# Optimization experiments

Hardware: AMD Instinct MI355X
Metric: run time of the kernel (lower is better)

## Reference

```python
import jax, jax.numpy as jnp
import numpy as np

N_NODES = 100000
N_EDGES = 1600000
NFEAT = 128
NHID = 128
NCLS = 40


def _glorot(key, shape):
    fan_in, fan_out = shape[1], shape[0]
    lim = (6.0 / (fan_in + fan_out)) ** 0.5
    return jax.random.uniform(key, shape, jnp.float32, -lim, lim)


def setup_inputs() -> dict:
    key = jax.random.key(0)
    ks = jax.random.split(key, 10)
    x = jax.random.normal(ks[0], (N_NODES, NFEAT), jnp.float32)
    edge_index = jax.random.randint(ks[1], (2, N_EDGES), 0, N_NODES, jnp.int64)
    return {
        "x": x,
        "edge_index": edge_index,
        # SAGEConv layer 0: lin_l (neighbor aggr, with bias) and lin_r (root)
        "W_l0": _glorot(ks[2], (NHID, NFEAT)),
        "b_l0": jnp.zeros((NHID,), jnp.float32),
        "W_r0": _glorot(ks[3], (NHID, NFEAT)),
        # SAGEConv layer 1
        "W_l1": _glorot(ks[4], (NHID, NHID)),
        "b_l1": jnp.zeros((NHID,), jnp.float32),
        "W_r1": _glorot(ks[5], (NHID, NHID)),
        # classifier
        "W_cls": _glorot(ks[6], (NCLS, NHID)),
        "b_cls": jnp.zeros((NCLS,), jnp.float32),
    }


def _sage_conv(x, src, dst, deg_inv, W_l, b_l, W_r):
    # gather source-node features along edges, mean-aggregate at targets
    msgs = x[src]                                            # [E, d_in]
    aggr = jax.ops.segment_sum(msgs, dst, num_segments=N_NODES)  # [N, d_in]
    aggr = aggr * deg_inv[:, None]                           # mean
    # out = lin_l(aggr) + lin_r(x)
    return aggr @ W_l.T + b_l + x @ W_r.T


def reference(x, edge_index, W_l0, b_l0, W_r0, W_l1, b_l1, W_r1, W_cls, b_cls):
    src, dst = edge_index[0], edge_index[1]
    deg = jax.ops.segment_sum(jnp.ones((src.shape[0],), x.dtype), dst,
                              num_segments=N_NODES)
    deg_inv = 1.0 / jnp.maximum(deg, 1.0)

    h = jax.nn.relu(_sage_conv(x, src, dst, deg_inv, W_l0, b_l0, W_r0))
    h = jax.nn.relu(_sage_conv(h, src, dst, deg_inv, W_l1, b_l1, W_r1))
    return h @ W_cls.T + b_cls  # [N, ncls]
```

## Files before the change

kernel.cpp:

```cpp
#include <hip/hip_runtime.h>

#define NN 100000
#define NE 1600000
#define DD 128
#define NCLS_ 40
#define PAD 64
#define NPART 8
#define PSZ 12500
#define PBLK 250
#define ECHUNK 6400

typedef unsigned short u16;
typedef unsigned int u32;
typedef __attribute__((ext_vector_type(8))) short short8;
typedef __attribute__((ext_vector_type(4))) float f32x4;

static __device__ __forceinline__ u16 f2b(float f) {
  u32 u = __float_as_uint(f);
  u32 r = (u + 0x7FFFu + ((u >> 16) & 1u)) >> 16;
  return (u16)r;
}

__global__ void k_flag(const int* __restrict__ ei, int* __restrict__ flag) {
  __shared__ int nz;
  if (threadIdx.x == 0) nz = 0;
  __syncthreads();
  if (threadIdx.x < 512) {
    int w = ei[2 * threadIdx.x + 1];
    if (w != 0) atomicOr(&nz, 1);
  }
  __syncthreads();
  if (threadIdx.x == 0) flag[0] = (nz == 0) ? 1 : 0;
}

static __device__ __forceinline__ int eget_nt(const int* ei, int pos, int is64) {
  return is64 ? __builtin_nontemporal_load(ei + 2 * (size_t)pos)
              : __builtin_nontemporal_load(ei + pos);
}

__global__ __launch_bounds__(256) void k_build(
    const int* __restrict__ ei, const int* __restrict__ flag,
    int* __restrict__ cnt, int* __restrict__ csrp) {
  int is64 = flag[0];
  int g = blockIdx.x & (NPART - 1);
  int sub = blockIdx.x >> 3;
  int e0 = sub * ECHUNK;
  int lo = g * PSZ;
  for (int e = e0 + threadIdx.x; e < e0 + ECHUNK; e += 256) {
    int dst = eget_nt(ei, NE + e, is64);
    if ((u32)(dst - lo) < (u32)PSZ) {
      int src = eget_nt(ei, e, is64);
      int r = atomicAdd(&cnt[dst], 1);
      if (r < PAD) csrp[dst * PAD + r] = src;
    }
  }
}

__global__ void k_cvt4(const float* __restrict__ s, u16* __restrict__ d, int n4) {
  int i = blockIdx.x * 256 + threadIdx.x;
  if (i >= n4) return;
  float4 v = ((const float4*)s)[i];
  u32 lo = (u32)f2b(v.x) | ((u32)f2b(v.y) << 16);
  u32 hi = (u32)f2b(v.z) | ((u32)f2b(v.w) << 16);
  ((uint2*)d)[i] = make_uint2(lo, hi);
}

__global__ void k_cvtw(const float* __restrict__ w0, const float* __restrict__ w1,
                       const float* __restrict__ w2, const float* __restrict__ w3,
                       u16* __restrict__ o0, u16* __restrict__ o1,
                       u16* __restrict__ o2, u16* __restrict__ o3) {
  int i = blockIdx.x * 256 + threadIdx.x;
  int which = i >> 12, j = i & 4095;
  const float* s = which == 0 ? w0 : which == 1 ? w1 : which == 2 ? w2 : w3;
  u16* d = which == 0 ? o0 : which == 1 ? o1 : which == 2 ? o2 : o3;
  float4 v = ((const float4*)s)[j];
  u32 lo = (u32)f2b(v.x) | ((u32)f2b(v.y) << 16);
  u32 hi = (u32)f2b(v.z) | ((u32)f2b(v.w) << 16);
  ((uint2*)d)[j] = make_uint2(lo, hi);
}

__global__ void k_cvtcls(const float* __restrict__ s, u16* __restrict__ d) {
  int i = blockIdx.x * 256 + threadIdx.x;
  if (i >= 48 * DD) return;
  float v = (i < NCLS_ * DD) ? s[i] : 0.f;
  d[i] = f2b(v);
}

__global__ __launch_bounds__(256, 2) void k_aggr(
    const u16* __restrict__ in, const int* __restrict__ csrp,
    const int* __restrict__ cnt, u16* __restrict__ out) {
  int wid = blockIdx.x * 4 + (threadIdx.x >> 6);
  if (wid >= NN) return;
  int lane = threadIdx.x & 63;
  int l16 = lane & 15;
  int deg = cnt[wid];
  int nb = deg > PAD ? PAD : deg;
  const u32* in32 = (const u32*)in;
  const int* seg = csrp + (size_t)wid * PAD;
  float a0 = 0.f, a1 = 0.f;
  int full = nb >> 4;
  for (int b = 0; b < full; b++) {
    int c = seg[b * 16 + l16];
    u32 v[16];
#pragma unroll
    for (int k = 0; k < 16; k++) {
      int sk = __builtin_amdgcn_readlane(c, k);
      v[k] = in32[(size_t)sk * 64 + lane];
    }
#pragma unroll
    for (int k = 0; k < 16; k++) {
      a0 += __uint_as_float(v[k] << 16);
      a1 += __uint_as_float(v[k] & 0xFFFF0000u);
    }
  }
  int done = full << 4;
  int rem = nb - done;
  if (rem) {
    int c = seg[done + (l16 < rem ? l16 : 0)];
    u32 v[16];
#pragma unroll
    for (int k = 0; k < 16; k++) {
      if (k < rem) {
        int sk = __builtin_amdgcn_readlane(c, k);
        v[k] = in32[(size_t)sk * 64 + lane];
      }
    }
#pragma unroll
    for (int k = 0; k < 16; k++) {
      if (k < rem) {
        a0 += __uint_as_float(v[k] << 16);
        a1 += __uint_as_float(v[k] & 0xFFFF0000u);
      }
    }
  }
  float sc = 1.0f / (float)(deg > 1 ? deg : 1);
  a0 *= sc;
  a1 *= sc;
  u32 pk = (u32)f2b(a0) | ((u32)f2b(a1) << 16);
  ((u32*)out)[(size_t)wid * 64 + lane] = pk;
}

template <int NT, bool RELU, bool F32OUT, bool HASR>
__global__ __launch_bounds__(256) void k_layer(
    const u16* A1, const u16* A2,
    const u16* __restrict__ WL, const u16* __restrict__ WR,
    const float* __restrict__ bias, void* out, int ncols) {
  int wv = blockIdx.x * 4 + (threadIdx.x >> 6);
  int base = wv * 16;
  if (base >= NN) return;
  int lane = threadIdx.x & 63;
  int m = lane & 15, kg = lane >> 4;
  f32x4 acc[NT];
#pragma unroll
  for (int t = 0; t < NT; t++) acc[t] = (f32x4){0.f, 0.f, 0.f, 0.f};
#pragma unroll
  for (int kk = 0; kk < 4; kk++) {
    int ko = kk * 32 + kg * 8;
    short8 aA = *(const short8*)(A1 + (size_t)(base + m) * DD + ko);
    short8 aX;
    if constexpr (HASR) aX = *(const short8*)(A2 + (size_t)(base + m) * DD + ko);
#pragma unroll
    for (int t = 0; t < NT; t++) {
      short8 bL = *(const short8*)(WL + (size_t)(t * 16 + m) * DD + ko);
      acc[t] = __builtin_amdgcn_mfma_f32_16x16x32_bf16(aA, bL, acc[t], 0, 0, 0);
      if constexpr (HASR) {
        short8 bR = *(const short8*)(WR + (size_t)(t * 16 + m) * DD + ko);
        acc[t] = __builtin_amdgcn_mfma_f32_16x16x32_bf16(aX, bR, acc[t], 0, 0, 0);
      }
    }
  }
#pragma unroll
  for (int t = 0; t < NT; t++) {
    int o = t * 16 + m;
#pragma unroll
    for (int r = 0; r < 4; r++) {
      int node = base + kg * 4 + r;
      float v = acc[t][r];
      if (o < ncols) v += bias[o];
      if constexpr (RELU) v = fmaxf(v, 0.f);
      if constexpr (F32OUT) {
        if (o < ncols) ((float*)out)[(size_t)node * ncols + o] = v;
      } else {
        ((u16*)out)[(size_t)node * DD + o] = f2b(v);
      }
    }
  }
}

extern "C" void kernel_launch(void* const* d_in, const int* in_sizes, int n_in,
                              void* d_out, int out_size, void* d_ws, size_t ws_size,
                              hipStream_t stream) {
  const float* x = (const float*)d_in[0];
  const int* ei = (const int*)d_in[1];
  const float* wl0 = (const float*)d_in[2];
  const float* bl0 = (const float*)d_in[3];
  const float* wr0 = (const float*)d_in[4];
  const float* wl1 = (const float*)d_in[5];
  const float* bl1 = (const float*)d_in[6];
  const float* wr1 = (const float*)d_in[7];
  const float* wcls = (const float*)d_in[8];
  const float* bcls = (const float*)d_in[9];

  char* ws = (char*)d_ws;
  size_t off = 0;
  auto alloc = [&](size_t b) {
    size_t r = off;
    off += (b + 255) & ~(size_t)255;
    return r;
  };
  int* flag = (int*)(ws + alloc(4));
  int* cnt = (int*)(ws + alloc((size_t)NN * 4));
  int* csrp = (int*)(ws + alloc((size_t)NN * PAD * 4));
  u16* xb = (u16*)(ws + alloc((size_t)NN * DD * 2));
  u16* h0 = (u16*)(ws + alloc((size_t)NN * DD * 2));
  u16* ag = (u16*)(ws + alloc((size_t)NN * DD * 2));
  u16* wl0b = (u16*)(ws + alloc((size_t)DD * DD * 2));
  u16* wr0b = (u16*)(ws + alloc((size_t)DD * DD * 2));
  u16* wl1b = (u16*)(ws + alloc((size_t)DD * DD * 2));
  u16* wr1b = (u16*)(ws + alloc((size_t)DD * DD * 2));
  u16* wclsb = (u16*)(ws + alloc((size_t)48 * DD * 2));
  if (off > ws_size) return;

  hipMemsetAsync(cnt, 0, (size_t)NN * 4, stream);
  k_flag<<<1, 512, 0, stream>>>(ei, flag);
  k_build<<<NPART * PBLK, 256, 0, stream>>>(ei, flag, cnt, csrp);

  k_cvt4<<<(NN * DD / 4 + 255) / 256, 256, 0, stream>>>(x, xb, NN * DD / 4);
  k_cvtw<<<64, 256, 0, stream>>>(wl0, wr0, wl1, wr1, wl0b, wr0b, wl1b, wr1b);
  k_cvtcls<<<(48 * DD + 255) / 256, 256, 0, stream>>>(wcls, wclsb);

  const int LB = (NN + 63) / 64;

  k_aggr<<<NN / 4, 256, 0, stream>>>(xb, csrp, cnt, ag);
  k_layer<8, true, false, true><<<LB, 256, 0, stream>>>(ag, xb, wl0b, wr0b, bl0, h0, DD);
  k_aggr<<<NN / 4, 256, 0, stream>>>(h0, csrp, cnt, ag);
  k_layer<8, true, false, true><<<LB, 256, 0, stream>>>(ag, h0, wl1b, wr1b, bl1, ag, DD);
  k_layer<3, false, true, false><<<LB, 256, 0, stream>>>(ag, nullptr, wclsb, nullptr, bcls, d_out, NCLS_);
}
```

Measured before the change: 359.4 us.

## Transpose padded CSR to slot-major and aggregate four nodes per wavefront

The padded neighbor table is now stored slot-major (slot r for all nodes contiguous), so the build kernel's scattered writes and the aggregation's index loads use a different layout. Each wavefront now processes four consecutive nodes, loading their degrees and 16 neighbor indices at once with int4 loads and issuing up to 64 independent row gathers per step for more memory-level parallelism. The cost is more registers (64 gathered values), divergence among the four nodes' degrees, and build writes strided by NN, which may scatter more across cache lines.

New measurement: 594.8 us. 65.5% more time.

```diff
diff --git a/kernel.cpp b/kernel.cpp
--- a/kernel.cpp
+++ b/kernel.cpp
@@ -51,7 +51,7 @@
     if ((u32)(dst - lo) < (u32)PSZ) {
       int src = eget_nt(ei, e, is64);
       int r = atomicAdd(&cnt[dst], 1);
-      if (r < PAD) csrp[dst * PAD + r] = src;
+      if (r < PAD) csrp[(size_t)r * NN + dst] = src;
     }
   }
 }
@@ -86,58 +86,50 @@
   d[i] = f2b(v);
 }
 
-__global__ __launch_bounds__(256, 2) void k_aggr(
+__global__ __launch_bounds__(256) void k_aggr(
     const u16* __restrict__ in, const int* __restrict__ csrp,
     const int* __restrict__ cnt, u16* __restrict__ out) {
-  int wid = blockIdx.x * 4 + (threadIdx.x >> 6);
-  if (wid >= NN) return;
+  int wv = threadIdx.x >> 6;
+  int base4 = blockIdx.x * 16 + wv * 4;
   int lane = threadIdx.x & 63;
   int l16 = lane & 15;
-  int deg = cnt[wid];
-  int nb = deg > PAD ? PAD : deg;
   const u32* in32 = (const u32*)in;
-  const int* seg = csrp + (size_t)wid * PAD;
-  float a0 = 0.f, a1 = 0.f;
-  int full = nb >> 4;
-  for (int b = 0; b < full; b++) {
-    int c = seg[b * 16 + l16];
-    u32 v[16];
+
+  int4 dv = *(const int4*)(cnt + base4);
+  int nb0 = dv.x > PAD ? PAD : dv.x;
+  int nb1 = dv.y > PAD ? PAD : dv.y;
+  int nb2 = dv.z > PAD ? PAD : dv.z;
+  int nb3 = dv.w > PAD ? PAD : dv.w;
+  int m01 = nb0 > nb1 ? nb0 : nb1, m23 = nb2 > nb3 ? nb2 : nb3;
+  int nbmax = m01 > m23 ? m01 : m23;
+
+  float a0[4] = {0.f, 0.f, 0.f, 0.f}, a1[4] = {0.f, 0.f, 0.f, 0.f};
+  for (int b = 0; b < nbmax; b += 16) {
+    int4 cv = *(const int4*)(csrp + (size_t)(b + l16) * NN + base4);
+    int rem0 = nb0 - b, rem1 = nb1 - b, rem2 = nb2 - b, rem3 = nb3 - b;
+    u32 v[4][16];
 #pragma unroll
     for (int k = 0; k < 16; k++) {
-      int sk = __builtin_amdgcn_readlane(c, k);
-      v[k] = in32[(size_t)sk * 64 + lane];
+      if (k < rem0) { int sk = __builtin_amdgcn_readlane(cv.x, k); v[0][k] = in32[(size_t)sk * 64 + lane]; }
+      if (k < rem1) { int sk = __builtin_amdgcn_readlane(cv.y, k); v[1][k] = in32[(size_t)sk * 64 + lane]; }
+      if (k < rem2) { int sk = __builtin_amdgcn_readlane(cv.z, k); v[2][k] = in32[(size_t)sk * 64 + lane]; }
+      if (k < rem3) { int sk = __builtin_amdgcn_readlane(cv.w, k); v[3][k] = in32[(size_t)sk * 64 + lane]; }
     }
 #pragma unroll
     for (int k = 0; k < 16; k++) {
-      a0 += __uint_as_float(v[k] << 16);
-      a1 += __uint_as_float(v[k] & 0xFFFF0000u);
-    }
-  }
-  int done = full << 4;
-  int rem = nb - done;
-  if (rem) {
-    int c = seg[done + (l16 < rem ? l16 : 0)];
-    u32 v[16];
-#pragma unroll
-    for (int k = 0; k < 16; k++) {
-      if (k < rem) {
-        int sk = __builtin_amdgcn_readlane(c, k);
-        v[k] = in32[(size_t)sk * 64 + lane];
-      }
-    }
-#pragma unroll
-    for (int k = 0; k < 16; k++) {
-      if (k < rem) {
-        a0 += __uint_as_float(v[k] << 16);
-        a1 += __uint_as_float(v[k] & 0xFFFF0000u);
-      }
-    }
-  }
-  float sc = 1.0f / (float)(deg > 1 ? deg : 1);
-  a0 *= sc;
-  a1 *= sc;
-  u32 pk = (u32)f2b(a0) | ((u32)f2b(a1) << 16);
-  ((u32*)out)[(size_t)wid * 64 + lane] = pk;
+      if (k < rem0) { a0[0] += __uint_as_float(v[0][k] << 16); a1[0] += __uint_as_float(v[0][k] & 0xFFFF0000u); }
+      if (k < rem1) { a0[1] += __uint_as_float(v[1][k] << 16); a1[1] += __uint_as_float(v[1][k] & 0xFFFF0000u); }
+      if (k < rem2) { a0[2] += __uint_as_float(v[2][k] << 16); a1[2] += __uint_as_float(v[2][k] & 0xFFFF0000u); }
+      if (k < rem3) { a0[3] += __uint_as_float(v[3][k] << 16); a1[3] += __uint_as_float(v[3][k] & 0xFFFF0000u); }
+    }
+  }
+  int degs[4] = {dv.x, dv.y, dv.z, dv.w};
+#pragma unroll
+  for (int j = 0; j < 4; j++) {
+    float sc = 1.0f / (float)(degs[j] > 1 ? degs[j] : 1);
+    u32 pk = (u32)f2b(a0[j] * sc) | ((u32)f2b(a1[j] * sc) << 16);
+    ((u32*)out)[(size_t)(base4 + j) * 64 + lane] = pk;
+  }
 }
 
 template <int NT, bool RELU, bool F32OUT, bool HASR>
@@ -230,10 +222,11 @@
   k_cvtcls<<<(48 * DD + 255) / 256, 256, 0, stream>>>(wcls, wclsb);
 
   const int LB = (NN + 63) / 64;
-
-  k_aggr<<<NN / 4, 256, 0, stream>>>(xb, csrp, cnt, ag);
+  const int AB = NN / 16;
+
+  k_aggr<<<AB, 256, 0, stream>>>(xb, csrp, cnt, ag);
   k_layer<8, true, false, true><<<LB, 256, 0, stream>>>(ag, xb, wl0b, wr0b, bl0, h0, DD);
-  k_aggr<<<NN / 4, 256, 0, stream>>>(h0, csrp, cnt, ag);
+  k_aggr<<<AB, 256, 0, stream>>>(h0, csrp, cnt, ag);
   k_layer<8, true, false, true><<<LB, 256, 0, stream>>>(ag, h0, wl1b, wr1b, bl1, ag, DD);
   k_layer<3, false, true, false><<<LB, 256, 0, stream>>>(ag, nullptr, wclsb, nullptr, bcls, d_out, NCLS_);
 }
```
